# Optimization experiments

Measured on AMD Instinct MI355X. Metric: run time of the kernel, lower is better.

The kernel has to match this reference:

```python
import jax, jax.numpy as jnp
import numpy as np

WINDOW_SIZE = 11
SIGMA = 1.5
C1 = 0.01 ** 2
C2 = 0.03 ** 2


def _gaussian_1d(window_size, sigma):
    x = np.arange(window_size, dtype=np.float32)
    g = np.exp(-((x - window_size // 2) ** 2) / (2.0 * sigma ** 2))
    g = g / g.sum()
    return jnp.asarray(g, dtype=jnp.float32)


def _blur(x, g1d):
    # Separable depthwise Gaussian blur, SAME padding.
    # x: [B, C, H, W]; mathematically identical to conv with outer(g, g).
    c = x.shape[1]
    pad = WINDOW_SIZE // 2
    kh = jnp.broadcast_to(g1d.reshape(1, 1, WINDOW_SIZE, 1), (c, 1, WINDOW_SIZE, 1))
    kw = jnp.broadcast_to(g1d.reshape(1, 1, 1, WINDOW_SIZE), (c, 1, 1, WINDOW_SIZE))
    dn = ('NCHW', 'OIHW', 'NCHW')
    x = jax.lax.conv_general_dilated(x, kh, (1, 1), [(pad, pad), (0, 0)],
                                     dimension_numbers=dn, feature_group_count=c)
    x = jax.lax.conv_general_dilated(x, kw, (1, 1), [(0, 0), (pad, pad)],
                                     dimension_numbers=dn, feature_group_count=c)
    return x


def setup_inputs() -> dict:
    key = jax.random.key(0)
    k1, k2 = jax.random.split(key)
    shape = (32, 1, 512, 512)
    img1 = jax.random.uniform(k1, shape, dtype=jnp.float32)
    img2 = jax.random.uniform(k2, shape, dtype=jnp.float32)
    return {"img1": img1, "img2": img2}


def reference(img1, img2):
    g1d = _gaussian_1d(WINDOW_SIZE, SIGMA)
    mu1 = _blur(img1, g1d)
    mu2 = _blur(img2, g1d)
    mu1_sq = mu1 * mu1
    mu2_sq = mu2 * mu2
    mu1_mu2 = mu1 * mu2
    sigma1_sq = _blur(img1 * img1, g1d) - mu1_sq
    sigma2_sq = _blur(img2 * img2, g1d) - mu2_sq
    sigma12 = _blur(img1 * img2, g1d) - mu1_mu2
    ssim_map = ((2.0 * mu1_mu2 + C1) * (2.0 * sigma12 + C2)) / (
        (mu1_sq + mu2_sq + C1) * (sigma1_sq + sigma2_sq + C2))
    return ssim_map.mean()  # size_average=True
```

## Files before the change

### kernel.cpp

```cpp
#include <hip/hip_runtime.h>

#define HH 512
#define WW 512
#define BATCH 32
#define BH 16
#define NB (HH / BH)
#define TPB 256
#define NBLOCKS (NB * BATCH)
#define PW 528
#define CBASE 0xAAAAAAAAu


typedef float f2 __attribute__((ext_vector_type(2)));

__global__ __launch_bounds__(TPB) void ssim_main(
    const float* __restrict__ img1,
    const float* __restrict__ img2,
    unsigned* __restrict__ counter,
    float* __restrict__ partial,
    float* __restrict__ out)
{
  constexpr float G[11] = {
      0.00102838f, 0.00759876f, 0.03600077f, 0.10936070f, 0.21300553f,
      0.26601171f,
      0.21300553f, 0.10936070f, 0.03600077f, 0.00759876f, 0.00102838f};
  constexpr float C1 = 1.0e-4f;
  constexpr float C2 = 9.0e-4f;

  const int tid  = threadIdx.x;
  const int band = blockIdx.x;
  const int bat  = blockIdx.y;
  const int r0   = band * BH;
  const float* p1 = img1 + (size_t)bat * (HH * WW);
  const float* p2 = img2 + (size_t)bat * (HH * WW);
  const int c0 = tid * 2;

  __shared__ __align__(16) float sp[4 * PW * 2];

  if (tid < 64) {
    const int a = tid >> 4, s = tid & 15;
    const int idx = (s < 9) ? s : (512 + s);
    *(f2*)(sp + a * (2 * PW) + 2 * idx) = f2{0.f, 0.f};
  }

  float2 w1[12], w2[12];
#pragma unroll
  for (int j = 0; j < 12; ++j) {
    const int r = r0 - 5 + j;
    float2 a = make_float2(0.f, 0.f), b = a;
    if (r >= 0 && r < HH) {
      a = *(const float2*)(p1 + r * WW + c0);
      b = *(const float2*)(p2 + r * WW + c0);
    }
    w1[j] = a; w2[j] = b;
  }

  __syncthreads();

  float ssum = 0.f;

#pragma unroll 1
  for (int q = 0; q < BH; q += 2) {
    float2 ta1 = make_float2(0.f, 0.f), ta2 = ta1, tb1 = ta1, tb2 = ta1;
    if (q + 2 < BH) {
      const int ra = r0 + 7 + q;
      const int rb = r0 + 8 + q;
      if (ra < HH) {
        ta1 = *(const float2*)(p1 + ra * WW + c0);
        ta2 = *(const float2*)(p2 + ra * WW + c0);
      }
      if (rb < HH) {
        tb1 = *(const float2*)(p1 + rb * WW + c0);
        tb2 = *(const float2*)(p2 + rb * WW + c0);
      }
    }

    f2 acc2[4][2];
#pragma unroll
    for (int a = 0; a < 4; ++a) { acc2[a][0] = f2{0.f, 0.f}; acc2[a][1] = f2{0.f, 0.f}; }

#pragma unroll
    for (int e = 0; e < 12; ++e) {
      const f2 g2 = f2{(e < 11) ? G[e] : 0.f, (e > 0) ? G[e - 1] : 0.f};
      const float xv[2] = {w1[e].x, w1[e].y};
      const float yv[2] = {w2[e].x, w2[e].y};
#pragma unroll
      for (int i = 0; i < 2; ++i) {
        const float x = xv[i], y = yv[i];
        const float s = fmaf(y, y, x * x);
        const float p = x * y;
        acc2[0][i] = __builtin_elementwise_fma(g2, f2{x, x}, acc2[0][i]);
        acc2[1][i] = __builtin_elementwise_fma(g2, f2{y, y}, acc2[1][i]);
        acc2[2][i] = __builtin_elementwise_fma(g2, f2{s, s}, acc2[2][i]);
        acc2[3][i] = __builtin_elementwise_fma(g2, f2{p, p}, acc2[3][i]);
      }
    }

#pragma unroll
    for (int a = 0; a < 4; ++a) {
      float* base = sp + a * (2 * PW) + 4 * tid + 18;
      *(f2*)(base)     = acc2[a][0];
      *(f2*)(base + 2) = acc2[a][1];
    }

    __syncthreads();

    f2 h2[4][2];
#pragma unroll
    for (int a = 0; a < 4; ++a) {
      const float* base = sp + a * (2 * PW);
      f2 t2[12];
#pragma unroll
      for (int m = 0; m < 6; ++m) {
        const float4 X = *(const float4*)(base + 4 * tid + 8 + 4 * m);
        t2[2 * m]     = f2{X.x, X.y};
        t2[2 * m + 1] = f2{X.z, X.w};
      }
#pragma unroll
      for (int j = 0; j < 2; ++j) {
        f2 hv = f2{0.f, 0.f};
#pragma unroll
        for (int k = 0; k < 11; ++k)
          hv = __builtin_elementwise_fma(f2{G[k], G[k]}, t2[j + k], hv);
        h2[a][j] = hv;
      }
    }

#pragma unroll
    for (int j = 0; j < 2; ++j) {
      const f2 mu1 = h2[0][j], mu2 = h2[1][j];
      const f2 S   = h2[2][j], P   = h2[3][j];
      const f2 mu12 = mu1 * mu2;
      const f2 den1 = __builtin_elementwise_fma(
          mu1, mu1, __builtin_elementwise_fma(mu2, mu2, f2{C1, C1}));
      const f2 vs   = S - den1 + f2{C1 + C2, C1 + C2};
      const f2 sg12 = P - mu12;
      const f2 num = (mu12 + mu12 + f2{C1, C1}) * (sg12 + sg12 + f2{C2, C2});
      const f2 den = den1 * vs;
      float rn0 = __builtin_amdgcn_rcpf(den.x);
      float rn1 = __builtin_amdgcn_rcpf(den.y);
      rn0 = rn0 * fmaf(-den.x, rn0, 2.0f);
      rn1 = rn1 * fmaf(-den.y, rn1, 2.0f);
      ssum = fmaf(num.x, rn0, ssum);
      ssum = fmaf(num.y, rn1, ssum);
    }

    __syncthreads();

#pragma unroll
    for (int j = 0; j < 10; ++j) { w1[j] = w1[j + 2]; w2[j] = w2[j + 2]; }
    w1[10] = ta1; w2[10] = ta2;
    w1[11] = tb1; w2[11] = tb2;
  }

#pragma unroll
  for (int off = 32; off > 0; off >>= 1) ssum += __shfl_xor(ssum, off, 64);
  float*  wred = sp;
  double* dred = (double*)(sp + 8);
  int*    flag = (int*)(sp + 16);
  const int wid = tid >> 6;
  if ((tid & 63) == 0) wred[wid] = ssum;
  __syncthreads();
  if (tid == 0) {
    const float bsum = wred[0] + wred[1] + wred[2] + wred[3];
    atomicExch(&partial[bat * NB + band], bsum);
    __threadfence();
    const unsigned old = atomicAdd(counter, 1u);
    flag[0] = (old == CBASE + (unsigned)NBLOCKS - 1u) ? 1 : 0;
  }
  __syncthreads();
  if (flag[0]) {
    double s = 0.0;
    for (int i = tid; i < NBLOCKS; i += TPB)
      s += (double)atomicAdd(&partial[i], 0.0f);
#pragma unroll
    for (int off = 32; off > 0; off >>= 1) s += __shfl_xor(s, off, 64);
    if ((tid & 63) == 0) dred[wid] = s;
    __syncthreads();
    if (tid == 0)
      out[0] = (float)((dred[0] + dred[1] + dred[2] + dred[3]) /
                       (double)((size_t)BATCH * HH * WW));
  }
}

extern "C" void kernel_launch(void* const* d_in, const int* in_sizes, int n_in,
                              void* d_out, int out_size, void* d_ws, size_t ws_size,
                              hipStream_t stream) {
  const float* img1 = (const float*)d_in[0];
  const float* img2 = (const float*)d_in[1];
  float* out = (float*)d_out;
  unsigned* counter = (unsigned*)d_ws;
  float* partial = (float*)((char*)d_ws + 16);
  dim3 grid(NB, BATCH);
  ssim_main<<<grid, TPB, 0, stream>>>(img1, img2, counter, partial, out);
}
```

Baseline: 124.4 us.

## Give each wavefront a private LDS strip with recomputed halo to drop barriers

Splits the shared horizontal-pass buffer into per-wavefront strips of 128 columns plus halo. Ten lanes per wave load the five halo columns on each side and redo their vertical blur, so each wave only reads LDS it wrote itself. This lets the kernel drop the block-wide __syncthreads calls inside the row loop. The cost is extra divergent scalar global loads and duplicated vertical-blur arithmetic for the halo lanes on every iteration. Correctness also relies on in-order LDS access within a wavefront, with no explicit wave-level fence.

```diff
diff --git a/kernel.cpp b/kernel.cpp
--- a/kernel.cpp
+++ b/kernel.cpp
@@ -7,7 +7,7 @@
 #define NB (HH / BH)
 #define TPB 256
 #define NBLOCKS (NB * BATCH)
-#define PW 528
+#define SLOTS 144
 #define CBASE 0xAAAAAAAAu
 
 
@@ -28,6 +28,8 @@
   constexpr float C2 = 9.0e-4f;
 
   const int tid  = threadIdx.x;
+  const int lane = tid & 63;
+  const int wv   = tid >> 6;
   const int band = blockIdx.x;
   const int bat  = blockIdx.y;
   const int r0   = band * BH;
@@ -35,13 +37,12 @@
   const float* p2 = img2 + (size_t)bat * (HH * WW);
   const int c0 = tid * 2;
 
-  __shared__ __align__(16) float sp[4 * PW * 2];
-
-  if (tid < 64) {
-    const int a = tid >> 4, s = tid & 15;
-    const int idx = (s < 9) ? s : (512 + s);
-    *(f2*)(sp + a * (2 * PW) + 2 * idx) = f2{0.f, 0.f};
-  }
+  __shared__ __align__(16) float sp[16 * 2 * SLOTS];
+
+  const int hcol  = (lane < 5) ? (128 * wv - 5 + lane)
+                               : (128 * wv + 128 + (lane - 5));
+  const int hslot = (lane < 5) ? (lane + 2) : (lane + 130);
+  const bool hcok = (hcol >= 0) && (hcol < WW);
 
   float2 w1[12], w2[12];
 #pragma unroll
@@ -54,8 +55,6 @@
     }
     w1[j] = a; w2[j] = b;
   }
-
-  __syncthreads();
 
   float ssum = 0.f;
 
@@ -75,10 +74,20 @@
       }
     }
 
+    float hx[12], hy[12];
+    if (lane < 10) {
+#pragma unroll
+      for (int j = 0; j < 12; ++j) {
+        const int r = r0 + q - 5 + j;
+        const bool ok = hcok && (r >= 0) && (r < HH);
+        hx[j] = ok ? p1[r * WW + hcol] : 0.f;
+        hy[j] = ok ? p2[r * WW + hcol] : 0.f;
+      }
+    }
+
     f2 acc2[4][2];
 #pragma unroll
     for (int a = 0; a < 4; ++a) { acc2[a][0] = f2{0.f, 0.f}; acc2[a][1] = f2{0.f, 0.f}; }
-
 #pragma unroll
     for (int e = 0; e < 12; ++e) {
       const f2 g2 = f2{(e < 11) ? G[e] : 0.f, (e > 0) ? G[e - 1] : 0.f};
@@ -96,23 +105,42 @@
       }
     }
 
+    if (lane < 10) {
+      f2 hacc[4];
+#pragma unroll
+      for (int a = 0; a < 4; ++a) hacc[a] = f2{0.f, 0.f};
+#pragma unroll
+      for (int e = 0; e < 12; ++e) {
+        const f2 g2 = f2{(e < 11) ? G[e] : 0.f, (e > 0) ? G[e - 1] : 0.f};
+        const float x = hx[e], y = hy[e];
+        const float s = fmaf(y, y, x * x);
+        const float p = x * y;
+        hacc[0] = __builtin_elementwise_fma(g2, f2{x, x}, hacc[0]);
+        hacc[1] = __builtin_elementwise_fma(g2, f2{y, y}, hacc[1]);
+        hacc[2] = __builtin_elementwise_fma(g2, f2{s, s}, hacc[2]);
+        hacc[3] = __builtin_elementwise_fma(g2, f2{p, p}, hacc[3]);
+      }
+#pragma unroll
+      for (int a = 0; a < 4; ++a)
+        *(f2*)(sp + (wv * 4 + a) * (2 * SLOTS) + 2 * hslot) = hacc[a];
+    }
+
 #pragma unroll
     for (int a = 0; a < 4; ++a) {
-      float* base = sp + a * (2 * PW) + 4 * tid + 18;
+      float* base = sp + (wv * 4 + a) * (2 * SLOTS) + 2 * (2 * lane + 7);
       *(f2*)(base)     = acc2[a][0];
       *(f2*)(base + 2) = acc2[a][1];
     }
 
-    __syncthreads();
 
     f2 h2[4][2];
 #pragma unroll
     for (int a = 0; a < 4; ++a) {
-      const float* base = sp + a * (2 * PW);
+      const float* base = sp + (wv * 4 + a) * (2 * SLOTS);
       f2 t2[12];
 #pragma unroll
       for (int m = 0; m < 6; ++m) {
-        const float4 X = *(const float4*)(base + 4 * tid + 8 + 4 * m);
+        const float4 X = *(const float4*)(base + 4 * lane + 4 + 4 * m);
         t2[2 * m]     = f2{X.x, X.y};
         t2[2 * m + 1] = f2{X.z, X.w};
       }
@@ -145,8 +173,6 @@
       ssum = fmaf(num.y, rn1, ssum);
     }
 
-    __syncthreads();
-
 #pragma unroll
     for (int j = 0; j < 10; ++j) { w1[j] = w1[j + 2]; w2[j] = w2[j + 2]; }
     w1[10] = ta1; w2[10] = ta2;
@@ -158,8 +184,7 @@
   float*  wred = sp;
   double* dred = (double*)(sp + 8);
   int*    flag = (int*)(sp + 16);
-  const int wid = tid >> 6;
-  if ((tid & 63) == 0) wred[wid] = ssum;
+  if (lane == 0) wred[wv] = ssum;
   __syncthreads();
   if (tid == 0) {
     const float bsum = wred[0] + wred[1] + wred[2] + wred[3];
@@ -175,7 +200,7 @@
       s += (double)atomicAdd(&partial[i], 0.0f);
 #pragma unroll
     for (int off = 32; off > 0; off >>= 1) s += __shfl_xor(s, off, 64);
-    if ((tid & 63) == 0) dred[wid] = s;
+    if (lane == 0) dred[wv] = s;
     __syncthreads();
     if (tid == 0)
       out[0] = (float)((dred[0] + dred[1] + dred[2] + dred[3]) /
```

After: 138.8 us. 11.6% more time.

## Process four columns per thread with 128-thread blocks and float4 loads

Applied to the files above, without the earlier changes.

Halves the threads per block and has each thread handle four adjacent columns instead of two, using float4 global loads and float4 shared-memory stores. The horizontal pass now reads a wider window per thread, so each shared-memory load is reused across more outputs and the halo overhead per output shrinks. The per-block and final reductions are cut down to two wavefronts to match. The cost is more registers per thread (larger row windows and accumulators) and half as many waves per block, which lowers occupancy and the latency hiding available on a grid that is already small.

```diff
diff --git a/kernel.cpp b/kernel.cpp
--- a/kernel.cpp
+++ b/kernel.cpp
@@ -5,7 +5,7 @@
 #define BATCH 32
 #define BH 16
 #define NB (HH / BH)
-#define TPB 256
+#define TPB 128
 #define NBLOCKS (NB * BATCH)
 #define PW 528
 #define CBASE 0xAAAAAAAAu
@@ -33,24 +33,24 @@
   const int r0   = band * BH;
   const float* p1 = img1 + (size_t)bat * (HH * WW);
   const float* p2 = img2 + (size_t)bat * (HH * WW);
-  const int c0 = tid * 2;
+  const int c0 = tid * 4;
 
   __shared__ __align__(16) float sp[4 * PW * 2];
 
   if (tid < 64) {
     const int a = tid >> 4, s = tid & 15;
-    const int idx = (s < 9) ? s : (512 + s);
+    const int idx = (s < 8) ? s : (512 + s);
     *(f2*)(sp + a * (2 * PW) + 2 * idx) = f2{0.f, 0.f};
   }
 
-  float2 w1[12], w2[12];
+  float4 w1[12], w2[12];
 #pragma unroll
   for (int j = 0; j < 12; ++j) {
     const int r = r0 - 5 + j;
-    float2 a = make_float2(0.f, 0.f), b = a;
+    float4 a = make_float4(0.f, 0.f, 0.f, 0.f), b = a;
     if (r >= 0 && r < HH) {
-      a = *(const float2*)(p1 + r * WW + c0);
-      b = *(const float2*)(p2 + r * WW + c0);
+      a = *(const float4*)(p1 + r * WW + c0);
+      b = *(const float4*)(p2 + r * WW + c0);
     }
     w1[j] = a; w2[j] = b;
   }
@@ -61,31 +61,33 @@
 
 #pragma unroll 1
   for (int q = 0; q < BH; q += 2) {
-    float2 ta1 = make_float2(0.f, 0.f), ta2 = ta1, tb1 = ta1, tb2 = ta1;
+    float4 ta1 = make_float4(0.f, 0.f, 0.f, 0.f), ta2 = ta1, tb1 = ta1, tb2 = ta1;
     if (q + 2 < BH) {
       const int ra = r0 + 7 + q;
       const int rb = r0 + 8 + q;
       if (ra < HH) {
-        ta1 = *(const float2*)(p1 + ra * WW + c0);
-        ta2 = *(const float2*)(p2 + ra * WW + c0);
+        ta1 = *(const float4*)(p1 + ra * WW + c0);
+        ta2 = *(const float4*)(p2 + ra * WW + c0);
       }
       if (rb < HH) {
-        tb1 = *(const float2*)(p1 + rb * WW + c0);
-        tb2 = *(const float2*)(p2 + rb * WW + c0);
-      }
-    }
-
-    f2 acc2[4][2];
-#pragma unroll
-    for (int a = 0; a < 4; ++a) { acc2[a][0] = f2{0.f, 0.f}; acc2[a][1] = f2{0.f, 0.f}; }
+        tb1 = *(const float4*)(p1 + rb * WW + c0);
+        tb2 = *(const float4*)(p2 + rb * WW + c0);
+      }
+    }
+
+    f2 acc2[4][4];
+#pragma unroll
+    for (int a = 0; a < 4; ++a)
+#pragma unroll
+      for (int i = 0; i < 4; ++i) acc2[a][i] = f2{0.f, 0.f};
 
 #pragma unroll
     for (int e = 0; e < 12; ++e) {
       const f2 g2 = f2{(e < 11) ? G[e] : 0.f, (e > 0) ? G[e - 1] : 0.f};
-      const float xv[2] = {w1[e].x, w1[e].y};
-      const float yv[2] = {w2[e].x, w2[e].y};
-#pragma unroll
-      for (int i = 0; i < 2; ++i) {
+      const float xv[4] = {w1[e].x, w1[e].y, w1[e].z, w1[e].w};
+      const float yv[4] = {w2[e].x, w2[e].y, w2[e].z, w2[e].w};
+#pragma unroll
+      for (int i = 0; i < 4; ++i) {
         const float x = xv[i], y = yv[i];
         const float s = fmaf(y, y, x * x);
         const float p = x * y;
@@ -98,36 +100,38 @@
 
 #pragma unroll
     for (int a = 0; a < 4; ++a) {
-      float* base = sp + a * (2 * PW) + 4 * tid + 18;
-      *(f2*)(base)     = acc2[a][0];
-      *(f2*)(base + 2) = acc2[a][1];
+      float* base = sp + a * (2 * PW) + 2 * (c0 + 8);
+      *(float4*)(base)     = make_float4(acc2[a][0].x, acc2[a][0].y,
+                                         acc2[a][1].x, acc2[a][1].y);
+      *(float4*)(base + 4) = make_float4(acc2[a][2].x, acc2[a][2].y,
+                                         acc2[a][3].x, acc2[a][3].y);
     }
 
     __syncthreads();
 
-    f2 h2[4][2];
+    f2 h2[4][4];
 #pragma unroll
     for (int a = 0; a < 4; ++a) {
       const float* base = sp + a * (2 * PW);
-      f2 t2[12];
-#pragma unroll
-      for (int m = 0; m < 6; ++m) {
-        const float4 X = *(const float4*)(base + 4 * tid + 8 + 4 * m);
+      f2 t2[16];
+#pragma unroll
+      for (int m = 0; m < 8; ++m) {
+        const float4 X = *(const float4*)(base + 8 * tid + 4 + 4 * m);
         t2[2 * m]     = f2{X.x, X.y};
         t2[2 * m + 1] = f2{X.z, X.w};
       }
 #pragma unroll
-      for (int j = 0; j < 2; ++j) {
+      for (int j = 0; j < 4; ++j) {
         f2 hv = f2{0.f, 0.f};
 #pragma unroll
         for (int k = 0; k < 11; ++k)
-          hv = __builtin_elementwise_fma(f2{G[k], G[k]}, t2[j + k], hv);
+          hv = __builtin_elementwise_fma(f2{G[k], G[k]}, t2[j + 1 + k], hv);
         h2[a][j] = hv;
       }
     }
 
 #pragma unroll
-    for (int j = 0; j < 2; ++j) {
+    for (int j = 0; j < 4; ++j) {
       const f2 mu1 = h2[0][j], mu2 = h2[1][j];
       const f2 S   = h2[2][j], P   = h2[3][j];
       const f2 mu12 = mu1 * mu2;
@@ -162,7 +166,7 @@
   if ((tid & 63) == 0) wred[wid] = ssum;
   __syncthreads();
   if (tid == 0) {
-    const float bsum = wred[0] + wred[1] + wred[2] + wred[3];
+    const float bsum = wred[0] + wred[1];
     atomicExch(&partial[bat * NB + band], bsum);
     __threadfence();
     const unsigned old = atomicAdd(counter, 1u);
@@ -178,7 +182,7 @@
     if ((tid & 63) == 0) dred[wid] = s;
     __syncthreads();
     if (tid == 0)
-      out[0] = (float)((dred[0] + dred[1] + dred[2] + dred[3]) /
+      out[0] = (float)((dred[0] + dred[1]) /
                        (double)((size_t)BATCH * HH * WW));
   }
 }
```

Result: slower. 138.2 us (+11.1%).
